# Kernel optimization log

Measured on AMD Instinct MI355X. Metric: run time of the kernel, lower is better.

The kernel has to match this reference:

```python
import jax, jax.numpy as jnp
import numpy as np

NUM_HEADS = 16
ROPE_BASE = 10000.0
EPS = 1e-6


def _rms_norm(x, scale):
    # RMSNorm over last dim with learnable scale (QKNorm over full `dim`).
    var = jnp.mean(jnp.square(x), axis=-1, keepdims=True)
    return x * jax.lax.rsqrt(var + EPS) * scale


def _rotate_half(x):
    x1, x2 = jnp.split(x, 2, axis=-1)
    return jnp.concatenate([-x2, x1], axis=-1)


def _apply_rope(q, k, rotary_dim):
    # q, k: (b, n, h, d); rotate first rotary_dim channels of each head.
    n = q.shape[1]
    half = rotary_dim // 2
    inv_freq = 1.0 / (ROPE_BASE ** (jnp.arange(0, half, dtype=jnp.float32) * 2.0 / rotary_dim))
    freqs = jnp.arange(n, dtype=jnp.float32)[:, None] * inv_freq[None, :]  # (n, half)
    emb = jnp.concatenate([freqs, freqs], axis=-1)  # (n, rotary_dim)
    cos = jnp.cos(emb)[None, :, None, :]
    sin = jnp.sin(emb)[None, :, None, :]

    def rot(x):
        x_rot, x_pass = x[..., :rotary_dim], x[..., rotary_dim:]
        x_rot = x_rot * cos + _rotate_half(x_rot) * sin
        return jnp.concatenate([x_rot, x_pass], axis=-1)

    return rot(q), rot(k)


def setup_inputs() -> dict:
    key = jax.random.key(0)
    ks = jax.random.split(key, 7)
    input_dim, dim = 1024, 1024
    b, n = 2, 2048
    s_in = 1.0 / np.sqrt(input_dim)
    s_d = 1.0 / np.sqrt(dim)
    return {
        "input": jax.random.normal(ks[0], (b, n, input_dim), dtype=jnp.float32),
        "w_qkv": jax.random.normal(ks[1], (input_dim, 3 * dim), dtype=jnp.float32) * s_in,
        "b_qkv": jax.random.normal(ks[2], (3 * dim,), dtype=jnp.float32) * 0.01,
        "q_scale": jnp.ones((dim,), dtype=jnp.float32) + 0.01 * jax.random.normal(ks[3], (dim,)),
        "k_scale": jnp.ones((dim,), dtype=jnp.float32) + 0.01 * jax.random.normal(ks[4], (dim,)),
        "w_out": jax.random.normal(ks[5], (dim, input_dim), dtype=jnp.float32) * s_d,
        "b_out": jax.random.normal(ks[6], (input_dim,), dtype=jnp.float32) * 0.01,
    }


def reference(input, w_qkv, b_qkv, q_scale, k_scale, w_out, b_out):
    b, n, _ = input.shape
    h = NUM_HEADS
    qkv = input @ w_qkv + b_qkv  # (b, n, 3*dim)
    q, k, v = jnp.split(qkv, 3, axis=-1)
    q = _rms_norm(q, q_scale)
    k = _rms_norm(k, k_scale)
    d = q.shape[-1] // h
    q = q.reshape(b, n, h, d)
    k = k.reshape(b, n, h, d)
    v = v.reshape(b, n, h, d)
    q, k = _apply_rope(q, k, rotary_dim=d)  # partial_rotary_factor=1
    scale = d ** (-0.5)
    attn = jnp.einsum("bqhd,bkhd->bhqk", q, k) * scale
    attn = jax.nn.softmax(attn, axis=-1)
    out = jnp.einsum("bhqk,bkhd->bqhd", attn, v).reshape(b, n, h * d)
    return out @ w_out + b_out
```

## Files before the change

kernel.cpp:

```cpp
#include <hip/hip_runtime.h>
#include <stdint.h>

typedef short bf16x8 __attribute__((ext_vector_type(8)));
typedef float f32x4 __attribute__((ext_vector_type(4)));
typedef float f32x16 __attribute__((ext_vector_type(16)));
typedef unsigned short u16;

#define MFMA_BF16 __builtin_amdgcn_mfma_f32_16x16x32_bf16
#define MFMA32 __builtin_amdgcn_mfma_f32_32x32x16_bf16
#define LOG2E 1.44269504088896f

#if __has_builtin(__builtin_amdgcn_exp2f)
#define EXP2(x) __builtin_amdgcn_exp2f(x)
#else
#define EXP2(x) exp2f(x)
#endif

static __device__ __forceinline__ u16 f2bf(float x) {
  union { float f; unsigned u; } v; v.f = x;
  unsigned r = v.u + 0x7fffu + ((v.u >> 16) & 1u);
  return (u16)(r >> 16);
}
static __device__ __forceinline__ float bf2f(u16 h) {
  union { unsigned u; float f; } v; v.u = ((unsigned)h) << 16; return v.f;
}
static __device__ __forceinline__ unsigned cvt_pk_bf16(float lo, float hi) {
  unsigned r;
  asm("v_cvt_pk_bf16_f32 %0, %1, %2" : "=v"(r) : "v"(lo), "v"(hi));
  return r;
}
static __device__ __forceinline__ void gld_lds16(const u16* g, u16* l) {
  __builtin_amdgcn_global_load_lds(
      (const __attribute__((address_space(1))) void*)g,
      (__attribute__((address_space(3))) void*)l, 16, 0, 0);
}

__global__ __launch_bounds__(256) void k_prep(const float* __restrict__ x,
                                              u16* __restrict__ y,
                                              const float* __restrict__ wqkv,
                                              u16* __restrict__ wqkvT,
                                              const float* __restrict__ wout,
                                              u16* __restrict__ woutT,
                                              float2* __restrict__ tab) {
  const int bid = blockIdx.x;
  const int tid = threadIdx.x;
  if (bid < 2048) {
    int i = bid * 256 + tid;
    const float4* p = (const float4*)x;
    float4 a = p[i * 2], b = p[i * 2 + 1];
    ushort4 o0, o1;
    o0.x = f2bf(a.x); o0.y = f2bf(a.y); o0.z = f2bf(a.z); o0.w = f2bf(a.w);
    o1.x = f2bf(b.x); o1.y = f2bf(b.y); o1.z = f2bf(b.z); o1.w = f2bf(b.w);
    ushort4* q = (ushort4*)y;
    q[i * 2] = o0; q[i * 2 + 1] = o1;
  } else if (bid < 3584) {
    int r = bid - 2048;
    int n = (r % 12) * 256 + tid;
    int k0 = (r / 12) * 8;
    u16 o[8];
#pragma unroll
    for (int j = 0; j < 8; j++) o[j] = f2bf(wqkv[(size_t)(k0 + j) * 3072 + n]);
    *(uint4*)&wqkvT[(size_t)n * 1024 + k0] = *(const uint4*)o;
  } else if (bid < 4096) {
    int r = bid - 3584;
    int n = (r % 4) * 256 + tid;
    int k0 = (r / 4) * 8;
    u16 o[8];
#pragma unroll
    for (int j = 0; j < 8; j++) o[j] = f2bf(wout[(size_t)(k0 + j) * 1024 + n]);
    *(uint4*)&woutT[(size_t)n * 1024 + k0] = *(const uint4*)o;
  } else {
    int i = (bid - 4096) * 256 + tid;
    int n = i >> 5, f = i & 31;
    float inv = exp2f(-(float)f * (13.287712379549449f / 32.f));
    float fr = (float)n * inv;
    float s, c;
    sincosf(fr, &s, &c);
    float2 cs; cs.x = c; cs.y = s;
    tab[i] = cs;
  }
}

template <int OUT_BF16>
__global__ __launch_bounds__(256, 2) void k_gemm(const u16* __restrict__ A,
                                                 const u16* __restrict__ Bt,
                                                 const float* __restrict__ bias,
                                                 void* __restrict__ Cp,
                                                 int M, int N, int K) {
  __shared__ u16 As[128 * 64];
  __shared__ u16 Bs[128 * 64];
  const int tid = threadIdx.x;
  const int lane = tid & 63;
  const int wid = tid >> 6;
  const int wm = wid >> 1, wn = wid & 1;
  const int m0 = blockIdx.x * 128, n0 = blockIdx.y * 128;

  const int sr = tid >> 3;
  const int sc = tid & 7;
  const int scsw = sc ^ (sr & 7);
  const u16* ga = A + (size_t)(m0 + sr) * K + (scsw << 3);
  const u16* gb = Bt + (size_t)(n0 + sr) * K + (scsw << 3);

  const int ar = wm * 64 + (lane & 15);
  const int br = wn * 64 + (lane & 15);
  const int cs0 = lane >> 4;

  f32x4 acc[4][4] = {};

  for (int k0 = 0; k0 < K; k0 += 64) {
    __syncthreads();
#pragma unroll
    for (int i = 0; i < 4; i++)
      gld_lds16(ga + k0 + i * (32 * K), &As[((tid & ~63) + 256 * i) * 8]);
#pragma unroll
    for (int i = 0; i < 4; i++)
      gld_lds16(gb + k0 + i * (32 * K), &Bs[((tid & ~63) + 256 * i) * 8]);
    __syncthreads();
#pragma unroll
    for (int kk = 0; kk < 2; kk++) {
      bf16x8 af[4], bfr[4];
#pragma unroll
      for (int mi = 0; mi < 4; mi++)
        af[mi] = *(const bf16x8*)&As[(ar + mi * 16) * 64 +
                                     (((kk * 4 + cs0) ^ (ar & 7)) << 3)];
#pragma unroll
      for (int ni = 0; ni < 4; ni++)
        bfr[ni] = *(const bf16x8*)&Bs[(br + ni * 16) * 64 +
                                      (((kk * 4 + cs0) ^ (br & 7)) << 3)];
#pragma unroll
      for (int mi = 0; mi < 4; mi++)
#pragma unroll
        for (int ni = 0; ni < 4; ni++)
          acc[mi][ni] = MFMA_BF16(af[mi], bfr[ni], acc[mi][ni], 0, 0, 0);
    }
  }

  const int crow0 = m0 + wm * 64 + ((lane >> 4) << 2);
  const int ccol0 = n0 + wn * 64 + (lane & 15);
#pragma unroll
  for (int ni = 0; ni < 4; ni++) {
    float bv = bias[ccol0 + ni * 16];
#pragma unroll
    for (int mi = 0; mi < 4; mi++) {
#pragma unroll
      for (int r = 0; r < 4; r++) {
        float v = acc[mi][ni][r] + bv;
        size_t idx = (size_t)(crow0 + mi * 16 + r) * N + ccol0 + ni * 16;
        if (OUT_BF16) ((u16*)Cp)[idx] = f2bf(v);
        else ((float*)Cp)[idx] = v;
      }
    }
  }
}

__global__ __launch_bounds__(256) void k_nv(const u16* __restrict__ qkv,
                                            const float* __restrict__ qscale,
                                            const float* __restrict__ kscale,
                                            const float2* __restrict__ tab,
                                            u16* __restrict__ Qb,
                                            u16* __restrict__ Kb,
                                            u16* __restrict__ Vt) {
  __shared__ __align__(16) u16 sm[64 * 72];
  const int t = threadIdx.x;
  if (blockIdx.x < 4096) {
    const int row = blockIdx.x;
    const int b = row >> 11, n = row & 2047;
    float* qn = (float*)sm;
    float* kn = qn + 1024;
    __shared__ float redq[4], redk[4];

    ushort4 q4 = *(const ushort4*)&qkv[(size_t)row * 3072 + t * 4];
    ushort4 k4 = *(const ushort4*)&qkv[(size_t)row * 3072 + 1024 + t * 4];
    float qv[4] = {bf2f(q4.x), bf2f(q4.y), bf2f(q4.z), bf2f(q4.w)};
    float kv[4] = {bf2f(k4.x), bf2f(k4.y), bf2f(k4.z), bf2f(k4.w)};
    float sq = 0.f, sk = 0.f;
#pragma unroll
    for (int j = 0; j < 4; j++) { sq += qv[j] * qv[j]; sk += kv[j] * kv[j]; }
#pragma unroll
    for (int o = 1; o < 64; o <<= 1) {
      sq += __shfl_xor(sq, o);
      sk += __shfl_xor(sk, o);
    }
    if ((t & 63) == 0) { redq[t >> 6] = sq; redk[t >> 6] = sk; }

    const int j0 = t * 4;
    const int d0 = j0 & 63;
    float2 cs[4];
    {
      const float2* tb = tab + n * 32 + (d0 & 31);
      *(float4*)&cs[0] = *(const float4*)&tb[0];
      *(float4*)&cs[2] = *(const float4*)&tb[2];
    }
    __syncthreads();
    float rq = rsqrtf((redq[0] + redq[1] + redq[2] + redq[3]) * (1.f / 1024.f) + 1e-6f);
    float rk = rsqrtf((redk[0] + redk[1] + redk[2] + redk[3]) * (1.f / 1024.f) + 1e-6f);
#pragma unroll
    for (int j = 0; j < 4; j++) {
      int jj = t * 4 + j;
      qn[jj] = qv[j] * rq * qscale[jj];
      kn[jj] = kv[j] * rk * kscale[jj];
    }
    __syncthreads();
    const int h = j0 >> 6;
    u16 qo[4], ko[4];
#pragma unroll
    for (int j = 0; j < 4; j++) {
      int jj = j0 + j;
      int dd = d0 + j;
      float c = cs[j].x, s = cs[j].y;
      float oq, ok;
      if (dd < 32) {
        oq = qn[jj] * c - qn[jj + 32] * s;
        ok = kn[jj] * c - kn[jj + 32] * s;
      } else {
        oq = qn[jj] * c + qn[jj - 32] * s;
        ok = kn[jj] * c + kn[jj - 32] * s;
      }
      qo[j] = f2bf(oq * (0.125f * LOG2E));
      ko[j] = f2bf(ok);
    }
    const size_t base = ((size_t)(b * 16 + h) * 2048 + n) * 64 + d0;
    *(ushort4*)&Qb[base] = *(const ushort4*)qo;
    *(ushort4*)&Kb[base] = *(const ushort4*)ko;
  } else {
    const int r = blockIdx.x - 4096;
    const int bh = r >> 5;
    const int b = bh >> 4, h = bh & 15;
    const int n0 = (r & 31) * 64;
    u16 (*tile)[72] = (u16(*)[72])sm;
#pragma unroll
    for (int i = 0; i < 2; i++) {
      int rr = (t >> 3) + 32 * i;
      int c = t & 7;
      uint4 v = *(const uint4*)&qkv[((size_t)(b * 2048 + n0 + rr)) * 3072 + 2048 + h * 64 + c * 8];
      *(uint4*)&tile[rr][c * 8] = v;
    }
    __syncthreads();
#pragma unroll
    for (int i = 0; i < 2; i++) {
      int dr = (t >> 3) + 32 * i;
      int c = t & 7;
      u16 vals[8];
#pragma unroll
      for (int j = 0; j < 8; j++) vals[j] = tile[c * 8 + j][dr];
      *(uint4*)&Vt[((size_t)bh * 64 + dr) * 2048 + n0 + c * 8] = *(const uint4*)vals;
    }
  }
}

__global__ __launch_bounds__(512, 4) void k_attn(const u16* __restrict__ Qb,
                                                 const u16* __restrict__ Kb,
                                                 const u16* __restrict__ Vt,
                                                 u16* __restrict__ Ob) {
  const int bh = blockIdx.y;
  const int q0 = blockIdx.x * 128;
  const int t = threadIdx.x, lane = t & 63, wid = t >> 6;
  const int grp = wid >> 2, sub = wid & 3;
  const int q = lane & 31, hi = lane >> 5;

  __shared__ u16 smem[32768];
  u16* Ks = smem;
  u16* Vs = smem + 4 * 4096;

  const u16* Qg = Qb + (size_t)bh * 2048 * 64;
  const u16* Kg = Kb + (size_t)bh * 2048 * 64;
  const u16* Vg = Vt + (size_t)bh * 64 * 2048;

  bf16x8 qf[4];
  {
    const u16* qrow = Qg + (size_t)(q0 + sub * 32 + q) * 64;
#pragma unroll
    for (int kk = 0; kk < 4; kk++)
      qf[kk] = *(const bf16x8*)&qrow[kk * 16 + hi * 8];
  }

  f32x16 ot[2] = {};
  float lacc[4] = {0.f, 0.f, 0.f, 0.f};

  const int srow = t >> 3;
  const int sslot = (t & 7) ^ (srow & 7);
  const u16* gk = Kg + srow * 64 + (sslot << 3);
  const u16* gv = Vg + (size_t)srow * 2048 + (sslot << 3);
  const int ldoff = (t & ~63) * 8;

#define STAGE(tile)                                                     \
  do {                                                                  \
    gld_lds16(gk + (size_t)(tile) * 4096, &Ks[((tile) & 3) * 4096 + ldoff]); \
    gld_lds16(gv + (size_t)(tile) * 64,   &Vs[((tile) & 3) * 4096 + ldoff]); \
  } while (0)

  STAGE(0); STAGE(1); STAGE(2); STAGE(3);

  for (int s = 0; s < 16; ++s) {
    if (s < 15) asm volatile("s_waitcnt vmcnt(4)" ::: "memory");
    else        asm volatile("s_waitcnt vmcnt(0)" ::: "memory");
    asm volatile("s_barrier" ::: "memory");

    const int myt = 2 * s + grp;
    const u16* Kc = &Ks[(myt & 3) * 4096];
    const u16* Vc = &Vs[(myt & 3) * 4096];

    f32x16 sv0 = {}, sv1 = {};
#pragma unroll
    for (int kk = 0; kk < 4; kk++) {
      const int kr0 = q;
      const int kr1 = 32 + q;
      bf16x8 kf0 = *(const bf16x8*)&Kc[kr0 * 64 + (((kk * 2 + hi) ^ (kr0 & 7)) << 3)];
      bf16x8 kf1 = *(const bf16x8*)&Kc[kr1 * 64 + (((kk * 2 + hi) ^ (kr1 & 7)) << 3)];
      __builtin_amdgcn_s_setprio(1);
      sv0 = MFMA32(kf0, qf[kk], sv0, 0, 0, 0);
      sv1 = MFMA32(kf1, qf[kk], sv1, 0, 0, 0);
      __builtin_amdgcn_s_setprio(0);
    }

    unsigned w[2][8];
#pragma unroll
    for (int i = 0; i < 8; i++) {
      float p0 = EXP2(sv0[2 * i]);
      float p1 = EXP2(sv0[2 * i + 1]);
      lacc[i & 3] += p0 + p1;
      w[0][i] = cvt_pk_bf16(p0, p1);
    }
#pragma unroll
    for (int i = 0; i < 8; i++) {
      float p0 = EXP2(sv1[2 * i]);
      float p1 = EXP2(sv1[2 * i + 1]);
      lacc[i & 3] += p0 + p1;
      w[1][i] = cvt_pk_bf16(p0, p1);
    }

#pragma unroll
    for (int ks = 0; ks < 4; ks++) {
      const int kvt = ks >> 1, i0 = (ks & 1) * 4;
      unsigned xs0 = hi ? w[kvt][i0 + 0] : w[kvt][i0 + 2];
      unsigned xs1 = hi ? w[kvt][i0 + 1] : w[kvt][i0 + 3];
      unsigned y0 = __shfl_xor(xs0, 32);
      unsigned y1 = __shfl_xor(xs1, 32);
      union { unsigned u[4]; bf16x8 v; } pf;
      pf.u[0] = hi ? y0 : w[kvt][i0 + 0];
      pf.u[1] = hi ? y1 : w[kvt][i0 + 1];
      pf.u[2] = hi ? w[kvt][i0 + 2] : y0;
      pf.u[3] = hi ? w[kvt][i0 + 3] : y1;
#pragma unroll
      for (int dt = 0; dt < 2; dt++) {
        const int vr = dt * 32 + q;
        bf16x8 va = *(const bf16x8*)&Vc[vr * 64 + (((ks * 2 + hi) ^ (vr & 7)) << 3)];
        __builtin_amdgcn_s_setprio(1);
        ot[dt] = MFMA32(va, pf.v, ot[dt], 0, 0, 0);
        __builtin_amdgcn_s_setprio(0);
      }
    }

    asm volatile("s_barrier" ::: "memory");
    if (s < 14) { STAGE(2 * s + 4); STAGE(2 * s + 5); }
  }
#undef STAGE

  float lsum = (lacc[0] + lacc[1]) + (lacc[2] + lacc[3]);
  lsum += __shfl_xor(lsum, 32);
  __syncthreads();
  float* obuf = (float*)smem;
  float* lbuf = (float*)(smem + 16384);
  if (grp == 1) {
    float* ob = obuf + (sub * 32 + q) * 64;
#pragma unroll
    for (int dt = 0; dt < 2; dt++)
#pragma unroll
      for (int g = 0; g < 4; g++) {
        float4 v4 = {ot[dt][4 * g], ot[dt][4 * g + 1], ot[dt][4 * g + 2], ot[dt][4 * g + 3]};
        *(float4*)&ob[dt * 32 + 8 * g + 4 * hi] = v4;
      }
    if (hi == 0) lbuf[sub * 32 + q] = lsum;
  }
  __syncthreads();
  if (grp == 0) {
    const float* ob = obuf + (sub * 32 + q) * 64;
    const float invl = 1.f / (lsum + lbuf[sub * 32 + q]);
    const int b = bh >> 4, h = bh & 15;
    const int rowq = q0 + sub * 32 + q;
    u16* orow = Ob + (size_t)(b * 2048 + rowq) * 1024 + h * 64;
#pragma unroll
    for (int dt = 0; dt < 2; dt++)
#pragma unroll
      for (int g = 0; g < 4; g++) {
        float4 v4 = *(const float4*)&ob[dt * 32 + 8 * g + 4 * hi];
        u16 o4[4];
        o4[0] = f2bf((ot[dt][4 * g + 0] + v4.x) * invl);
        o4[1] = f2bf((ot[dt][4 * g + 1] + v4.y) * invl);
        o4[2] = f2bf((ot[dt][4 * g + 2] + v4.z) * invl);
        o4[3] = f2bf((ot[dt][4 * g + 3] + v4.w) * invl);
        *(ushort4*)&orow[dt * 32 + 8 * g + 4 * hi] = *(const ushort4*)o4;
      }
  }
}

extern "C" void kernel_launch(void* const* d_in, const int* in_sizes, int n_in,
                              void* d_out, int out_size, void* d_ws, size_t ws_size,
                              hipStream_t stream) {
  const float* input = (const float*)d_in[0];
  const float* w_qkv = (const float*)d_in[1];
  const float* b_qkv = (const float*)d_in[2];
  const float* q_scale = (const float*)d_in[3];
  const float* k_scale = (const float*)d_in[4];
  const float* w_out = (const float*)d_in[5];
  const float* b_out = (const float*)d_in[6];
  float* out = (float*)d_out;

  char* ws = (char*)d_ws;
  u16* Abuf  = (u16*)(ws);
  u16* WqkvT = (u16*)(ws + 8388608);
  u16* WoutT = (u16*)(ws + 14680064);
  u16* qkv   = (u16*)(ws + 16777216);
  u16* Qb    = (u16*)(ws + 41943040);
  u16* Kb    = (u16*)(ws + 50331648);
  u16* Vt    = (u16*)(ws + 58720256);
  u16* Attn  = (u16*)(ws + 67108864);
  float2* Rt = (float2*)(ws + 75497472);

  k_prep<<<4352, 256, 0, stream>>>(input, Abuf, w_qkv, WqkvT, w_out, WoutT, Rt);
  k_gemm<1><<<dim3(32, 24), 256, 0, stream>>>(Abuf, WqkvT, b_qkv, qkv, 4096, 3072, 1024);
  k_nv<<<5120, 256, 0, stream>>>(qkv, q_scale, k_scale, Rt, Qb, Kb, Vt);
  k_attn<<<dim3(16, 32), 512, 0, stream>>>(Qb, Kb, Vt, Attn);
  k_gemm<0><<<dim3(32, 8), 256, 0, stream>>>(Attn, WoutT, b_out, out, 4096, 1024, 1024);
}
```

Baseline: 122.4 us.

## Split attention KV across four wave groups with 64-query blocks

The attention kernel now handles 64 queries per block instead of 128 and splits the KV sequence across four wave groups that each work on 32-key tiles. The partial outputs are merged with a two-level tree reduction through shared memory. Launching twice as many blocks with half the LDS is meant to raise occupancy and CU utilisation. In exchange, each block issues twice as many K/V loads per query and waits on vmcnt(0) every step, which removes the overlap between prefetch and compute and adds extra synchronisations.

After: 391.1 us. +219.4%, slower.

```diff
diff --git a/kernel.cpp b/kernel.cpp
--- a/kernel.cpp
+++ b/kernel.cpp
@@ -248,19 +248,20 @@
   }
 }
 
-__global__ __launch_bounds__(512, 4) void k_attn(const u16* __restrict__ Qb,
+__global__ __launch_bounds__(512, 8) void k_attn(const u16* __restrict__ Qb,
                                                  const u16* __restrict__ Kb,
                                                  const u16* __restrict__ Vt,
                                                  u16* __restrict__ Ob) {
   const int bh = blockIdx.y;
-  const int q0 = blockIdx.x * 128;
+  const int q0 = blockIdx.x * 64;
   const int t = threadIdx.x, lane = t & 63, wid = t >> 6;
-  const int grp = wid >> 2, sub = wid & 3;
+  const int grp = wid >> 1, sub = wid & 1;
   const int q = lane & 31, hi = lane >> 5;
 
-  __shared__ u16 smem[32768];
+  __shared__ __align__(16) u16 smem[16384];
+  __shared__ float lA[64], lB[64], lC[64];
   u16* Ks = smem;
-  u16* Vs = smem + 4 * 4096;
+  u16* Vs = smem + 8192;
 
   const u16* Qg = Qb + (size_t)bh * 2048 * 64;
   const u16* Kg = Kb + (size_t)bh * 2048 * 64;
@@ -277,74 +278,59 @@
   f32x16 ot[2] = {};
   float lacc[4] = {0.f, 0.f, 0.f, 0.f};
 
-  const int srow = t >> 3;
-  const int sslot = (t & 7) ^ (srow & 7);
-  const u16* gk = Kg + srow * 64 + (sslot << 3);
-  const u16* gv = Vg + (size_t)srow * 2048 + (sslot << 3);
-  const int ldoff = (t & ~63) * 8;
-
-#define STAGE(tile)                                                     \
-  do {                                                                  \
-    gld_lds16(gk + (size_t)(tile) * 4096, &Ks[((tile) & 3) * 4096 + ldoff]); \
-    gld_lds16(gv + (size_t)(tile) * 64,   &Vs[((tile) & 3) * 4096 + ldoff]); \
-  } while (0)
+  const int t2 = t & 255;
+  const bool isK = wid < 4;
+  const u16* gsrc = isK
+      ? Kg + (size_t)(t2 >> 3) * 64 + (((t2 & 7) ^ ((t2 >> 3) & 7)) << 3)
+      : Vg + (size_t)(t2 >> 2) * 2048 + (((t2 & 3) ^ ((t2 >> 2) & 3)) << 3);
+  const size_t gstep = isK ? 2048 : 32;
+  u16* lbase = (isK ? Ks : Vs) + (t2 & ~63) * 8;
+
+#define STAGE(tile) gld_lds16(gsrc + (size_t)(tile) * gstep, lbase + ((tile) & 3) * 2048)
 
   STAGE(0); STAGE(1); STAGE(2); STAGE(3);
 
+  const u16* Kc = &Ks[grp * 2048];
+  const u16* Vc = &Vs[grp * 2048];
+
   for (int s = 0; s < 16; ++s) {
-    if (s < 15) asm volatile("s_waitcnt vmcnt(4)" ::: "memory");
-    else        asm volatile("s_waitcnt vmcnt(0)" ::: "memory");
+    asm volatile("s_waitcnt vmcnt(0)" ::: "memory");
     asm volatile("s_barrier" ::: "memory");
 
-    const int myt = 2 * s + grp;
-    const u16* Kc = &Ks[(myt & 3) * 4096];
-    const u16* Vc = &Vs[(myt & 3) * 4096];
-
-    f32x16 sv0 = {}, sv1 = {};
+    f32x16 sv = {};
 #pragma unroll
     for (int kk = 0; kk < 4; kk++) {
-      const int kr0 = q;
-      const int kr1 = 32 + q;
-      bf16x8 kf0 = *(const bf16x8*)&Kc[kr0 * 64 + (((kk * 2 + hi) ^ (kr0 & 7)) << 3)];
-      bf16x8 kf1 = *(const bf16x8*)&Kc[kr1 * 64 + (((kk * 2 + hi) ^ (kr1 & 7)) << 3)];
+      bf16x8 kf = *(const bf16x8*)&Kc[q * 64 + (((kk * 2 + hi) ^ (q & 7)) << 3)];
       __builtin_amdgcn_s_setprio(1);
-      sv0 = MFMA32(kf0, qf[kk], sv0, 0, 0, 0);
-      sv1 = MFMA32(kf1, qf[kk], sv1, 0, 0, 0);
+      sv = MFMA32(kf, qf[kk], sv, 0, 0, 0);
       __builtin_amdgcn_s_setprio(0);
     }
 
-    unsigned w[2][8];
+    unsigned w[8];
 #pragma unroll
     for (int i = 0; i < 8; i++) {
-      float p0 = EXP2(sv0[2 * i]);
-      float p1 = EXP2(sv0[2 * i + 1]);
+      float p0 = EXP2(sv[2 * i]);
+      float p1 = EXP2(sv[2 * i + 1]);
       lacc[i & 3] += p0 + p1;
-      w[0][i] = cvt_pk_bf16(p0, p1);
-    }
-#pragma unroll
-    for (int i = 0; i < 8; i++) {
-      float p0 = EXP2(sv1[2 * i]);
-      float p1 = EXP2(sv1[2 * i + 1]);
-      lacc[i & 3] += p0 + p1;
-      w[1][i] = cvt_pk_bf16(p0, p1);
-    }
-
-#pragma unroll
-    for (int ks = 0; ks < 4; ks++) {
-      const int kvt = ks >> 1, i0 = (ks & 1) * 4;
-      unsigned xs0 = hi ? w[kvt][i0 + 0] : w[kvt][i0 + 2];
-      unsigned xs1 = hi ? w[kvt][i0 + 1] : w[kvt][i0 + 3];
+      w[i] = cvt_pk_bf16(p0, p1);
+    }
+
+#pragma unroll
+    for (int ks = 0; ks < 2; ks++) {
+      const int i0 = ks * 4;
+      unsigned xs0 = hi ? w[i0 + 0] : w[i0 + 2];
+      unsigned xs1 = hi ? w[i0 + 1] : w[i0 + 3];
       unsigned y0 = __shfl_xor(xs0, 32);
       unsigned y1 = __shfl_xor(xs1, 32);
       union { unsigned u[4]; bf16x8 v; } pf;
-      pf.u[0] = hi ? y0 : w[kvt][i0 + 0];
-      pf.u[1] = hi ? y1 : w[kvt][i0 + 1];
-      pf.u[2] = hi ? w[kvt][i0 + 2] : y0;
-      pf.u[3] = hi ? w[kvt][i0 + 3] : y1;
+      pf.u[0] = hi ? y0 : w[i0 + 0];
+      pf.u[1] = hi ? y1 : w[i0 + 1];
+      pf.u[2] = hi ? w[i0 + 2] : y0;
+      pf.u[3] = hi ? w[i0 + 3] : y1;
 #pragma unroll
       for (int dt = 0; dt < 2; dt++) {
         const int vr = dt * 32 + q;
-        bf16x8 va = *(const bf16x8*)&Vc[vr * 64 + (((ks * 2 + hi) ^ (vr & 7)) << 3)];
+        bf16x8 va = *(const bf16x8*)&Vc[vr * 32 + (((ks * 2 + hi) ^ (vr & 3)) << 3)];
         __builtin_amdgcn_s_setprio(1);
         ot[dt] = MFMA32(va, pf.v, ot[dt], 0, 0, 0);
         __builtin_amdgcn_s_setprio(0);
@@ -352,46 +338,76 @@
     }
 
     asm volatile("s_barrier" ::: "memory");
-    if (s < 14) { STAGE(2 * s + 4); STAGE(2 * s + 5); }
+    if (s < 15) { STAGE(4 * s + 4); STAGE(4 * s + 5); STAGE(4 * s + 6); STAGE(4 * s + 7); }
   }
 #undef STAGE
 
   float lsum = (lacc[0] + lacc[1]) + (lacc[2] + lacc[3]);
   lsum += __shfl_xor(lsum, 32);
+
   __syncthreads();
-  float* obuf = (float*)smem;
-  float* lbuf = (float*)(smem + 16384);
-  if (grp == 1) {
-    float* ob = obuf + (sub * 32 + q) * 64;
-#pragma unroll
-    for (int dt = 0; dt < 2; dt++)
-#pragma unroll
-      for (int g = 0; g < 4; g++) {
-        float4 v4 = {ot[dt][4 * g], ot[dt][4 * g + 1], ot[dt][4 * g + 2], ot[dt][4 * g + 3]};
-        *(float4*)&ob[dt * 32 + 8 * g + 4 * hi] = v4;
-      }
-    if (hi == 0) lbuf[sub * 32 + q] = lsum;
-  }
+  float* slotA = (float*)smem;
+  float* slotB = (float*)(smem + 8192);
+  const int row = sub * 32 + q;
+
+#define DUMP(slot, lv)                                                        \
+  do {                                                                        \
+    float* ob = (slot) + row * 64;                                            \
+    _Pragma("unroll")                                                         \
+    for (int dt = 0; dt < 2; dt++)                                            \
+      _Pragma("unroll")                                                       \
+      for (int g = 0; g < 4; g++) {                                           \
+        float4 v4 = {ot[dt][4 * g], ot[dt][4 * g + 1], ot[dt][4 * g + 2],     \
+                     ot[dt][4 * g + 3]};                                      \
+        *(float4*)&ob[dt * 32 + 8 * g + 4 * hi] = v4;                         \
+      }                                                                       \
+    if (lane < 32) (lv)[row] = lsum;                                          \
+  } while (0)
+
+#define ACCUM(slot, lv)                                                       \
+  do {                                                                        \
+    const float* ob = (slot) + row * 64;                                      \
+    _Pragma("unroll")                                                         \
+    for (int dt = 0; dt < 2; dt++)                                            \
+      _Pragma("unroll")                                                       \
+      for (int g = 0; g < 4; g++) {                                           \
+        float4 v4 = *(const float4*)&ob[dt * 32 + 8 * g + 4 * hi];            \
+        ot[dt][4 * g + 0] += v4.x;                                            \
+        ot[dt][4 * g + 1] += v4.y;                                            \
+        ot[dt][4 * g + 2] += v4.z;                                            \
+        ot[dt][4 * g + 3] += v4.w;                                            \
+      }                                                                       \
+    lsum += (lv)[row];                                                        \
+  } while (0)
+
+  if (grp == 1) DUMP(slotA, lA);
+  if (grp == 3) DUMP(slotB, lB);
+  __syncthreads();
+  if (grp == 0) ACCUM(slotA, lA);
+  if (grp == 2) ACCUM(slotB, lB);
+  __syncthreads();
+  if (grp == 2) DUMP(slotA, lC);
   __syncthreads();
   if (grp == 0) {
-    const float* ob = obuf + (sub * 32 + q) * 64;
-    const float invl = 1.f / (lsum + lbuf[sub * 32 + q]);
+    ACCUM(slotA, lC);
+    const float invl = 1.f / lsum;
     const int b = bh >> 4, h = bh & 15;
-    const int rowq = q0 + sub * 32 + q;
+    const int rowq = q0 + row;
     u16* orow = Ob + (size_t)(b * 2048 + rowq) * 1024 + h * 64;
 #pragma unroll
     for (int dt = 0; dt < 2; dt++)
 #pragma unroll
       for (int g = 0; g < 4; g++) {
-        float4 v4 = *(const float4*)&ob[dt * 32 + 8 * g + 4 * hi];
         u16 o4[4];
-        o4[0] = f2bf((ot[dt][4 * g + 0] + v4.x) * invl);
-        o4[1] = f2bf((ot[dt][4 * g + 1] + v4.y) * invl);
-        o4[2] = f2bf((ot[dt][4 * g + 2] + v4.z) * invl);
-        o4[3] = f2bf((ot[dt][4 * g + 3] + v4.w) * invl);
+        o4[0] = f2bf(ot[dt][4 * g + 0] * invl);
+        o4[1] = f2bf(ot[dt][4 * g + 1] * invl);
+        o4[2] = f2bf(ot[dt][4 * g + 2] * invl);
+        o4[3] = f2bf(ot[dt][4 * g + 3] * invl);
         *(ushort4*)&orow[dt * 32 + 8 * g + 4 * hi] = *(const ushort4*)o4;
       }
   }
+#undef DUMP
+#undef ACCUM
 }
 
 extern "C" void kernel_launch(void* const* d_in, const int* in_sizes, int n_in,
@@ -420,6 +436,6 @@
   k_prep<<<4352, 256, 0, stream>>>(input, Abuf, w_qkv, WqkvT, w_out, WoutT, Rt);
   k_gemm<1><<<dim3(32, 24), 256, 0, stream>>>(Abuf, WqkvT, b_qkv, qkv, 4096, 3072, 1024);
   k_nv<<<5120, 256, 0, stream>>>(qkv, q_scale, k_scale, Rt, Qb, Kb, Vt);
-  k_attn<<<dim3(16, 32), 512, 0, stream>>>(Qb, Kb, Vt, Attn);
+  k_attn<<<dim3(32, 32), 512, 0, stream>>>(Qb, Kb, Vt, Attn);
   k_gemm<0><<<dim3(32, 8), 256, 0, stream>>>(Attn, WoutT, b_out, out, 4096, 1024, 1024);
 }
```

## Halve attention KV tile to 32 keys to shrink LDS and raise occupancy

Applied to the files above, without the earlier changes.

Reduces each staged K/V tile in the attention kernel from 64 to 32 keys, cutting shared memory from 64KB to about 33KB so more blocks can reside per CU. The loop count doubles to 32 steps. Loading is restructured so half the threads stage K and the other half stage V, with the XOR swizzle adapted to the narrower V rows. The aim is to hide latency through more resident blocks, at the cost of twice as many barriers and waits and fewer MFMAs between synchronizations.

After: 124.7 us. No clear change (+1.9%).

```diff
diff --git a/kernel.cpp b/kernel.cpp
--- a/kernel.cpp
+++ b/kernel.cpp
@@ -258,9 +258,9 @@
   const int grp = wid >> 2, sub = wid & 3;
   const int q = lane & 31, hi = lane >> 5;
 
-  __shared__ u16 smem[32768];
+  __shared__ __align__(16) u16 smem[16384 + 256];
   u16* Ks = smem;
-  u16* Vs = smem + 4 * 4096;
+  u16* Vs = smem + 8192;
 
   const u16* Qg = Qb + (size_t)bh * 2048 * 64;
   const u16* Kg = Kb + (size_t)bh * 2048 * 64;
@@ -277,74 +277,61 @@
   f32x16 ot[2] = {};
   float lacc[4] = {0.f, 0.f, 0.f, 0.f};
 
-  const int srow = t >> 3;
-  const int sslot = (t & 7) ^ (srow & 7);
-  const u16* gk = Kg + srow * 64 + (sslot << 3);
-  const u16* gv = Vg + (size_t)srow * 2048 + (sslot << 3);
-  const int ldoff = (t & ~63) * 8;
-
-#define STAGE(tile)                                                     \
-  do {                                                                  \
-    gld_lds16(gk + (size_t)(tile) * 4096, &Ks[((tile) & 3) * 4096 + ldoff]); \
-    gld_lds16(gv + (size_t)(tile) * 64,   &Vs[((tile) & 3) * 4096 + ldoff]); \
-  } while (0)
+  const int t2 = t & 255;
+  const bool isK = t < 256;
+  const u16* gsrc = isK
+      ? Kg + (size_t)(t2 >> 3) * 64 + (((t2 & 7) ^ ((t2 >> 3) & 7)) << 3)
+      : Vg + (size_t)(t2 >> 2) * 2048 + (((t2 & 3) ^ ((t2 >> 2) & 3)) << 3);
+  const size_t gstep = isK ? 2048 : 32;
+  u16* lbase = (isK ? Ks : Vs) + (t2 & ~63) * 8;
+
+#define STAGE(tile) gld_lds16(gsrc + (size_t)(tile) * gstep, lbase + ((tile) & 3) * 2048)
 
   STAGE(0); STAGE(1); STAGE(2); STAGE(3);
 
-  for (int s = 0; s < 16; ++s) {
-    if (s < 15) asm volatile("s_waitcnt vmcnt(4)" ::: "memory");
+  for (int s = 0; s < 32; ++s) {
+    if (s < 31) asm volatile("s_waitcnt vmcnt(2)" ::: "memory");
     else        asm volatile("s_waitcnt vmcnt(0)" ::: "memory");
     asm volatile("s_barrier" ::: "memory");
 
     const int myt = 2 * s + grp;
-    const u16* Kc = &Ks[(myt & 3) * 4096];
-    const u16* Vc = &Vs[(myt & 3) * 4096];
-
-    f32x16 sv0 = {}, sv1 = {};
+    const u16* Kc = &Ks[(myt & 3) * 2048];
+    const u16* Vc = &Vs[(myt & 3) * 2048];
+
+    f32x16 sv = {};
 #pragma unroll
     for (int kk = 0; kk < 4; kk++) {
-      const int kr0 = q;
-      const int kr1 = 32 + q;
-      bf16x8 kf0 = *(const bf16x8*)&Kc[kr0 * 64 + (((kk * 2 + hi) ^ (kr0 & 7)) << 3)];
-      bf16x8 kf1 = *(const bf16x8*)&Kc[kr1 * 64 + (((kk * 2 + hi) ^ (kr1 & 7)) << 3)];
+      bf16x8 kf = *(const bf16x8*)&Kc[q * 64 + (((kk * 2 + hi) ^ (q & 7)) << 3)];
       __builtin_amdgcn_s_setprio(1);
-      sv0 = MFMA32(kf0, qf[kk], sv0, 0, 0, 0);
-      sv1 = MFMA32(kf1, qf[kk], sv1, 0, 0, 0);
+      sv = MFMA32(kf, qf[kk], sv, 0, 0, 0);
       __builtin_amdgcn_s_setprio(0);
     }
 
-    unsigned w[2][8];
+    unsigned w[8];
 #pragma unroll
     for (int i = 0; i < 8; i++) {
-      float p0 = EXP2(sv0[2 * i]);
-      float p1 = EXP2(sv0[2 * i + 1]);
+      float p0 = EXP2(sv[2 * i]);
+      float p1 = EXP2(sv[2 * i + 1]);
       lacc[i & 3] += p0 + p1;
-      w[0][i] = cvt_pk_bf16(p0, p1);
-    }
-#pragma unroll
-    for (int i = 0; i < 8; i++) {
-      float p0 = EXP2(sv1[2 * i]);
-      float p1 = EXP2(sv1[2 * i + 1]);
-      lacc[i & 3] += p0 + p1;
-      w[1][i] = cvt_pk_bf16(p0, p1);
-    }
-
-#pragma unroll
-    for (int ks = 0; ks < 4; ks++) {
-      const int kvt = ks >> 1, i0 = (ks & 1) * 4;
-      unsigned xs0 = hi ? w[kvt][i0 + 0] : w[kvt][i0 + 2];
-      unsigned xs1 = hi ? w[kvt][i0 + 1] : w[kvt][i0 + 3];
+      w[i] = cvt_pk_bf16(p0, p1);
+    }
+
+#pragma unroll
+    for (int ks = 0; ks < 2; ks++) {
+      const int i0 = ks * 4;
+      unsigned xs0 = hi ? w[i0 + 0] : w[i0 + 2];
+      unsigned xs1 = hi ? w[i0 + 1] : w[i0 + 3];
       unsigned y0 = __shfl_xor(xs0, 32);
       unsigned y1 = __shfl_xor(xs1, 32);
       union { unsigned u[4]; bf16x8 v; } pf;
-      pf.u[0] = hi ? y0 : w[kvt][i0 + 0];
-      pf.u[1] = hi ? y1 : w[kvt][i0 + 1];
-      pf.u[2] = hi ? w[kvt][i0 + 2] : y0;
-      pf.u[3] = hi ? w[kvt][i0 + 3] : y1;
+      pf.u[0] = hi ? y0 : w[i0 + 0];
+      pf.u[1] = hi ? y1 : w[i0 + 1];
+      pf.u[2] = hi ? w[i0 + 2] : y0;
+      pf.u[3] = hi ? w[i0 + 3] : y1;
 #pragma unroll
       for (int dt = 0; dt < 2; dt++) {
         const int vr = dt * 32 + q;
-        bf16x8 va = *(const bf16x8*)&Vc[vr * 64 + (((ks * 2 + hi) ^ (vr & 7)) << 3)];
+        bf16x8 va = *(const bf16x8*)&Vc[vr * 32 + (((ks * 2 + hi) ^ (vr & 3)) << 3)];
         __builtin_amdgcn_s_setprio(1);
         ot[dt] = MFMA32(va, pf.v, ot[dt], 0, 0, 0);
         __builtin_amdgcn_s_setprio(0);
@@ -352,17 +339,19 @@
     }
 
     asm volatile("s_barrier" ::: "memory");
-    if (s < 14) { STAGE(2 * s + 4); STAGE(2 * s + 5); }
+    if (s < 30) { STAGE(2 * s + 4); STAGE(2 * s + 5); }
   }
 #undef STAGE
 
   float lsum = (lacc[0] + lacc[1]) + (lacc[2] + lacc[3]);
   lsum += __shfl_xor(lsum, 32);
+
   __syncthreads();
   float* obuf = (float*)smem;
   float* lbuf = (float*)(smem + 16384);
+  const int row = sub * 32 + q;
   if (grp == 1) {
-    float* ob = obuf + (sub * 32 + q) * 64;
+    float* ob = obuf + row * 64;
 #pragma unroll
     for (int dt = 0; dt < 2; dt++)
 #pragma unroll
@@ -370,14 +359,14 @@
         float4 v4 = {ot[dt][4 * g], ot[dt][4 * g + 1], ot[dt][4 * g + 2], ot[dt][4 * g + 3]};
         *(float4*)&ob[dt * 32 + 8 * g + 4 * hi] = v4;
       }
-    if (hi == 0) lbuf[sub * 32 + q] = lsum;
+    if (hi == 0) lbuf[row] = lsum;
   }
   __syncthreads();
   if (grp == 0) {
-    const float* ob = obuf + (sub * 32 + q) * 64;
-    const float invl = 1.f / (lsum + lbuf[sub * 32 + q]);
+    const float* ob = obuf + row * 64;
+    const float invl = 1.f / (lsum + lbuf[row]);
     const int b = bh >> 4, h = bh & 15;
-    const int rowq = q0 + sub * 32 + q;
+    const int rowq = q0 + row;
     u16* orow = Ob + (size_t)(b * 2048 + rowq) * 1024 + h * 64;
 #pragma unroll
     for (int dt = 0; dt < 2; dt++)
```
